# Kernel optimization log

Hardware: AMD Instinct MI355X
Metric: run time of the kernel (lower is better)

The kernel has to match this reference:

```python
import jax, jax.numpy as jnp
import numpy as np

N = 50000
E = 800000
F_IN = 64
F_OUT = 64


def setup_inputs() -> dict:
    key = jax.random.key(0)
    ks = jax.random.split(key, 14)
    x = jax.random.normal(ks[0], (N, F_IN), dtype=jnp.float32)
    row_low = jax.random.randint(ks[1], (E,), 0, N)
    col_low = jax.random.randint(ks[2], (E,), 0, N)
    val_low = jax.random.uniform(ks[3], (E,), dtype=jnp.float32)
    row_high = jax.random.randint(ks[4], (E,), 0, N)
    col_high = jax.random.randint(ks[5], (E,), 0, N)
    val_high = jax.random.uniform(ks[6], (E,), dtype=jnp.float32)
    # xavier-uniform style init for weights
    def xavier(k, shape):
        fan_in, fan_out = shape[0], shape[1]
        bound = float(np.sqrt(6.0 / (fan_in + fan_out)))
        return jax.random.uniform(k, shape, jnp.float32, -bound, bound)
    W_low = xavier(ks[7], (F_IN, F_OUT))
    W_high = xavier(ks[8], (F_IN, F_OUT))
    W_mlp = xavier(ks[9], (F_IN, F_OUT))
    a_low = xavier(ks[10], (F_OUT, 1))
    a_high = xavier(ks[11], (F_OUT, 1))
    a_mlp = xavier(ks[12], (F_OUT, 1))
    att3 = xavier(ks[13], (3, 3))
    return dict(x=x, row_low=row_low, col_low=col_low, val_low=val_low,
                row_high=row_high, col_high=col_high, val_high=val_high,
                W_low=W_low, W_high=W_high, W_mlp=W_mlp,
                a_low=a_low, a_high=a_high, a_mlp=a_mlp, att3=att3)


def _spmm(row, col, val, h, n):
    # (sparse adj) @ h : gather source rows, scale by edge weight, scatter-add to dest
    return jax.ops.segment_sum(val[:, None] * h[col], row, num_segments=n)


def reference(x, row_low, col_low, val_low, row_high, col_high, val_high,
              W_low, W_high, W_mlp, a_low, a_high, a_mlp, att3):
    n = x.shape[0]
    out_low = jax.nn.relu(_spmm(row_low, col_low, val_low, x @ W_low, n))
    out_high = jax.nn.relu(_spmm(row_high, col_high, val_high, x @ W_high, n))
    out_mlp = jax.nn.relu(x @ W_mlp)
    T = 3.0
    feats = jnp.concatenate([out_low @ a_low, out_high @ a_high, out_mlp @ a_mlp], axis=1)  # [N,3]
    logits = (jax.nn.sigmoid(feats) @ att3) / T
    att = jax.nn.softmax(logits, axis=1)  # [N,3]
    return 3.0 * (att[:, 0:1] * out_low + att[:, 1:2] * out_high + att[:, 2:3] * out_mlp)
```

## Files before the change

kernel.cpp:

```cpp
#include <hip/hip_runtime.h>
#include <hip/hip_fp16.h>


#define NNODE 50000
#define NEDGE 800000
#define NBUCK 782
#define CAP   1552

typedef __attribute__((ext_vector_type(8))) short short8v;
typedef __attribute__((ext_vector_type(4))) float float4v;

__device__ __forceinline__ unsigned short f2bf(float f) {
    unsigned u = __float_as_uint(f);
    u += 0x7FFFu + ((u >> 16) & 1u);
    return (unsigned short)(u >> 16);
}
__device__ __forceinline__ __half2 u_as_h2(unsigned u) {
    return *reinterpret_cast<__half2*>(&u);
}

__global__ __launch_bounds__(256)
void zero_kernel(unsigned int* __restrict__ g)
{
    const int i = blockIdx.x * 256 + threadIdx.x;
    if (i < 2 * NBUCK) g[i] = 0u;
}

__global__ __launch_bounds__(256)
void gemm_mfma_kernel(const float* __restrict__ x,
                      const float* __restrict__ Wl, const float* __restrict__ Wh,
                      const float* __restrict__ Wm,
                      unsigned short* __restrict__ hl16,
                      unsigned short* __restrict__ hh16,
                      unsigned short* __restrict__ hm16)
{
    __shared__ unsigned short wt[3][64][72];
    const int t = threadIdx.x;
#pragma unroll 1
    for (int m = 0; m < 3; ++m) {
        const float* __restrict__ W = (m == 0) ? Wl : (m == 1) ? Wh : Wm;
        for (int i = t; i < 4096; i += 256) {
            const int k = i >> 6, c = i & 63;
            wt[m][c][k] = f2bf(W[i]);
        }
    }
    __syncthreads();

    const int wid = t >> 6, lane = t & 63;
    const int node0 = blockIdx.x * 64 + wid * 16;
    if (node0 >= NNODE) return;
    const int arow = lane & 15;
    const int hi = lane >> 4;

    const float* __restrict__ xr = x + (size_t)(node0 + arow) * 64 + hi * 8;
    const float4 pa0 = *(const float4*)(xr + 0);
    const float4 pa1 = *(const float4*)(xr + 4);
    const float4 pb0 = *(const float4*)(xr + 32);
    const float4 pb1 = *(const float4*)(xr + 36);
    short8v a0, a1;
    a0[0] = (short)f2bf(pa0.x); a0[1] = (short)f2bf(pa0.y);
    a0[2] = (short)f2bf(pa0.z); a0[3] = (short)f2bf(pa0.w);
    a0[4] = (short)f2bf(pa1.x); a0[5] = (short)f2bf(pa1.y);
    a0[6] = (short)f2bf(pa1.z); a0[7] = (short)f2bf(pa1.w);
    a1[0] = (short)f2bf(pb0.x); a1[1] = (short)f2bf(pb0.y);
    a1[2] = (short)f2bf(pb0.z); a1[3] = (short)f2bf(pb0.w);
    a1[4] = (short)f2bf(pb1.x); a1[5] = (short)f2bf(pb1.y);
    a1[6] = (short)f2bf(pb1.z); a1[7] = (short)f2bf(pb1.w);

#pragma unroll 1
    for (int m = 0; m < 3; ++m) {
        unsigned short* __restrict__ H = (m == 0) ? hl16 : (m == 1) ? hh16 : hm16;
        float4v acc0 = {0.f, 0.f, 0.f, 0.f}, acc1 = {0.f, 0.f, 0.f, 0.f};
        float4v acc2 = {0.f, 0.f, 0.f, 0.f}, acc3 = {0.f, 0.f, 0.f, 0.f};

#define DO_CT(CT, ACC)                                                          \
        {                                                                       \
            const short8v b0 = *(const short8v*)&wt[m][CT * 16 + arow][hi * 8]; \
            const short8v b1 = *(const short8v*)&wt[m][CT * 16 + arow][32 + hi * 8]; \
            ACC = __builtin_amdgcn_mfma_f32_16x16x32_bf16(a0, b0, ACC, 0, 0, 0); \
            ACC = __builtin_amdgcn_mfma_f32_16x16x32_bf16(a1, b1, ACC, 0, 0, 0); \
        }
        DO_CT(0, acc0) DO_CT(1, acc1) DO_CT(2, acc2) DO_CT(3, acc3)
#undef DO_CT

        const bool rl = (m == 2);
#define ST_CT(CT, ACC)                                                          \
        {                                                                       \
            _Pragma("unroll")                                                   \
            for (int r = 0; r < 4; ++r) {                                       \
                float v = ACC[r];                                               \
                if (rl) v = fmaxf(v, 0.f);                                      \
                H[(size_t)(node0 + hi * 4 + r) * 64 + CT * 16 + arow] =         \
                    __half_as_ushort(__float2half(v));                          \
            }                                                                   \
        }
        ST_CT(0, acc0) ST_CT(1, acc1) ST_CT(2, acc2) ST_CT(3, acc3)
#undef ST_CT
    }
}

__global__ __launch_bounds__(512)
void scatter_kernel(const int* __restrict__ row_low, const int* __restrict__ col_low,
                    const float* __restrict__ val_low,
                    const int* __restrict__ row_high, const int* __restrict__ col_high,
                    const float* __restrict__ val_high,
                    unsigned int* __restrict__ gcursor, uint2* __restrict__ packed)
{
    __shared__ unsigned int hist_s[2 * NBUCK];
    __shared__ unsigned int base_s[2 * NBUCK];
    const int t = threadIdx.x;
    const int ebase = blockIdx.x * 8192;

    for (int i = t; i < 2 * NBUCK; i += 512) hist_s[i] = 0u;
    __syncthreads();

    int rows[16]; unsigned int rank[16];
#pragma unroll
    for (int j = 0; j < 16; ++j) {
        const int e = ebase + j * 512 + t;
        rows[j] = 0; rank[j] = 0u;
        if (e < 2 * NEDGE) {
            const int r = (e < NEDGE) ? row_low[e] : row_high[e - NEDGE];
            const int fb = ((e < NEDGE) ? 0 : NBUCK) + (r >> 6);
            rows[j] = r;
            rank[j] = atomicAdd(&hist_s[fb], 1u);
        }
    }
    __syncthreads();
    for (int i = t; i < 2 * NBUCK; i += 512) {
        const unsigned int c = hist_s[i];
        base_s[i] = c ? atomicAdd(&gcursor[i], c) : 0u;
    }
    __syncthreads();
#pragma unroll
    for (int j = 0; j < 16; ++j) {
        const int e = ebase + j * 512 + t;
        if (e < 2 * NEDGE) {
            const int g = (e >= NEDGE);
            const int ee = e - g * NEDGE;
            const int r = rows[j];
            const int c = g ? col_high[ee] : col_low[ee];
            const float v = g ? val_high[ee] : val_low[ee];
            const int fb = g * NBUCK + (r >> 6);
            const unsigned int pos = base_s[fb] + rank[j];
            if (pos < CAP) {
                const unsigned short hb = __half_as_ushort(__float2half(v));
                uint2 pk;
                pk.x = (unsigned int)c | ((unsigned int)(r & 63) << 16);
                pk.y = (unsigned)hb | ((unsigned)hb << 16);
                packed[(size_t)fb * CAP + pos] = pk;
            }
        }
    }
}

__global__ __launch_bounds__(256)
void sort_kernel(uint2* __restrict__ packed,
                 const unsigned int* __restrict__ gcursor,
                 int* __restrict__ rs, int* __restrict__ rc)
{
    __shared__ uint2 es[CAP];
    __shared__ unsigned int hist[64];
    __shared__ unsigned int offs[64];
    __shared__ unsigned int cur[64];

    const int fb = blockIdx.x;
    const int t = threadIdx.x;
    uint2* __restrict__ seg = packed + (size_t)fb * CAP;
    int cnt = (int)gcursor[fb];
    if (cnt > CAP) cnt = CAP;

    if (t < 64) { hist[t] = 0u; cur[t] = 0u; }
    __syncthreads();

    for (int i = t; i < cnt; i += 256) {
        const uint2 p = seg[i];
        es[i] = p;
        atomicAdd(&hist[(p.x >> 16) & 63u], 1u);
    }
    __syncthreads();

    if (t < 64) {
        const int pv = (int)((hist[t] + 7u) & ~7u);
        int xsc = pv;
#pragma unroll
        for (int d = 1; d < 64; d <<= 1) {
            int y = __shfl_up(xsc, d, 64);
            if (t >= d) xsc += y;
        }
        offs[t] = (unsigned)(xsc - pv);
    }
    __syncthreads();

    for (int i = t; i < cnt; i += 256) {
        const uint2 p = es[i];
        const unsigned r = (p.x >> 16) & 63u;
        const unsigned pos = offs[r] + atomicAdd(&cur[r], 1u);
        if (pos < CAP) seg[pos] = p;
    }
    if (t < 64) {
        const unsigned b = offs[t] + hist[t];
        const unsigned e = offs[t] + ((hist[t] + 7u) & ~7u);
        const uint2 z = {0u, 0u};
        for (unsigned u = b; u < e && u < CAP; ++u) seg[u] = z;
    }

    if (t < 64) {
        const int g = (fb >= NBUCK);
        const int node = ((fb - g * NBUCK) << 6) + t;
        if (node < NNODE) {
            const unsigned P = (hist[t] + 7u) & ~7u;
            const int avail = CAP - (int)offs[t];
            int nq = (int)(P >> 2);
            int nqa = avail > 0 ? ((avail >> 2) & ~1) : 0;
            if (nq > nqa) nq = nqa;
            rs[g * NNODE + node] = fb * CAP + (int)offs[t];
            rc[g * NNODE + node] = nq;
        }
    }
}

__global__ __launch_bounds__(256, 8)
void spmm_finalize_kernel(const uint2* __restrict__ packed,
                          const int* __restrict__ rs, const int* __restrict__ rc,
                          const unsigned short* __restrict__ hl16,
                          const unsigned short* __restrict__ hh16,
                          const unsigned short* __restrict__ hm16,
                          const float* __restrict__ aL, const float* __restrict__ aH,
                          const float* __restrict__ aM, const float* __restrict__ att3,
                          float* __restrict__ out)
{
    const int wid = threadIdx.x >> 6;
    const int lane = threadIdx.x & 63;
    const int sub = lane >> 4;
    const int f4 = (lane & 15) << 2;
    const unsigned fb2 = (unsigned)(f4 * 2);
    const int node = blockIdx.x * 4 + wid;
    if (node >= NNODE) return;

    const int sL = __builtin_amdgcn_readfirstlane(rs[node]);
    const int nqL = __builtin_amdgcn_readfirstlane(rc[node]);
    const int sH = __builtin_amdgcn_readfirstlane(rs[NNODE + node]);
    const int nqH = __builtin_amdgcn_readfirstlane(rc[NNODE + node]);
    const uint2* __restrict__ segL = packed + sL + sub;
    const uint2* __restrict__ segH = packed + sH + sub;
    const int nqm = (nqL > nqH) ? nqL : nqH;

    const __half2 hz2 = u_as_h2(0u);
    __half2 aL0a = hz2, aL1a = hz2, aL0b = hz2, aL1b = hz2;
    __half2 aH0a = hz2, aH1a = hz2, aH0b = hz2, aH1b = hz2;

    uint2 cL0 = segL[0], cL1 = segL[4];
    uint2 cH0 = segH[0], cH1 = segH[4];

#pragma unroll 1
    for (int q = 0; q < nqm; q += 2) {
        const uint2 nL0 = segL[q * 4 + 8],  nL1 = segL[q * 4 + 12];
        const uint2 nH0 = segH[q * 4 + 8],  nH1 = segH[q * 4 + 12];
        const uint2 uL0 = *(const uint2*)((const char*)hl16 + (size_t)(((cL0.x & 0xFFFFu) << 7) + fb2));
        const uint2 uL1 = *(const uint2*)((const char*)hl16 + (size_t)(((cL1.x & 0xFFFFu) << 7) + fb2));
        const uint2 uH0 = *(const uint2*)((const char*)hh16 + (size_t)(((cH0.x & 0xFFFFu) << 7) + fb2));
        const uint2 uH1 = *(const uint2*)((const char*)hh16 + (size_t)(((cH1.x & 0xFFFFu) << 7) + fb2));
        __builtin_amdgcn_sched_barrier(0);
        const __half2 vL0 = u_as_h2((q     < nqL) ? cL0.y : 0u);
        const __half2 vL1 = u_as_h2((q + 1 < nqL) ? cL1.y : 0u);
        const __half2 vH0 = u_as_h2((q     < nqH) ? cH0.y : 0u);
        const __half2 vH1 = u_as_h2((q + 1 < nqH) ? cH1.y : 0u);
        aL0a = __hfma2(u_as_h2(uL0.x), vL0, aL0a);
        aL1a = __hfma2(u_as_h2(uL0.y), vL0, aL1a);
        aL0b = __hfma2(u_as_h2(uL1.x), vL1, aL0b);
        aL1b = __hfma2(u_as_h2(uL1.y), vL1, aL1b);
        aH0a = __hfma2(u_as_h2(uH0.x), vH0, aH0a);
        aH1a = __hfma2(u_as_h2(uH0.y), vH0, aH1a);
        aH0b = __hfma2(u_as_h2(uH1.x), vH1, aH0b);
        aH1b = __hfma2(u_as_h2(uH1.y), vH1, aH1b);
        cL0 = nL0; cL1 = nL1; cH0 = nH0; cH1 = nH1;
    }

    float lx = __low2float(aL0a) + __low2float(aL0b);
    float ly = __high2float(aL0a) + __high2float(aL0b);
    float lz = __low2float(aL1a) + __low2float(aL1b);
    float lw = __high2float(aL1a) + __high2float(aL1b);
    float hx = __low2float(aH0a) + __low2float(aH0b);
    float hy = __high2float(aH0a) + __high2float(aH0b);
    float hz = __low2float(aH1a) + __low2float(aH1b);
    float hw = __high2float(aH1a) + __high2float(aH1b);

    lx += __shfl_xor(lx, 16, 64); ly += __shfl_xor(ly, 16, 64);
    lz += __shfl_xor(lz, 16, 64); lw += __shfl_xor(lw, 16, 64);
    hx += __shfl_xor(hx, 16, 64); hy += __shfl_xor(hy, 16, 64);
    hz += __shfl_xor(hz, 16, 64); hw += __shfl_xor(hw, 16, 64);
    lx += __shfl_xor(lx, 32, 64); ly += __shfl_xor(ly, 32, 64);
    lz += __shfl_xor(lz, 32, 64); lw += __shfl_xor(lw, 32, 64);
    hx += __shfl_xor(hx, 32, 64); hy += __shfl_xor(hy, 32, 64);
    hz += __shfl_xor(hz, 32, 64); hw += __shfl_xor(hw, 32, 64);

    const float olx = fmaxf(lx, 0.f), oly = fmaxf(ly, 0.f);
    const float olz = fmaxf(lz, 0.f), olw = fmaxf(lw, 0.f);
    const float ohx = fmaxf(hx, 0.f), ohy = fmaxf(hy, 0.f);
    const float ohz = fmaxf(hz, 0.f), ohw = fmaxf(hw, 0.f);

    const uint2 om2 = *(const uint2*)&hm16[(size_t)node * 64 + f4];
    const float omx = __low2float(u_as_h2(om2.x));
    const float omy = __high2float(u_as_h2(om2.x));
    const float omz = __low2float(u_as_h2(om2.y));
    const float omw = __high2float(u_as_h2(om2.y));

    const float4 aL4 = *(const float4*)&aL[f4];
    const float4 aH4 = *(const float4*)&aH[f4];
    const float4 aM4 = *(const float4*)&aM[f4];

    float f0 = olx * aL4.x + oly * aL4.y + olz * aL4.z + olw * aL4.w;
    float f1 = ohx * aH4.x + ohy * aH4.y + ohz * aH4.z + ohw * aH4.w;
    float f2 = omx * aM4.x + omy * aM4.y + omz * aM4.z + omw * aM4.w;
#pragma unroll
    for (int msk = 1; msk < 16; msk <<= 1) {
        f0 += __shfl_xor(f0, msk, 64);
        f1 += __shfl_xor(f1, msk, 64);
        f2 += __shfl_xor(f2, msk, 64);
    }
    const float s0 = 1.f / (1.f + __expf(-f0));
    const float s1 = 1.f / (1.f + __expf(-f1));
    const float s2 = 1.f / (1.f + __expf(-f2));
    const float invT = 1.f / 3.f;
    const float l0g = (s0 * att3[0] + s1 * att3[3] + s2 * att3[6]) * invT;
    const float l1g = (s0 * att3[1] + s1 * att3[4] + s2 * att3[7]) * invT;
    const float l2g = (s0 * att3[2] + s1 * att3[5] + s2 * att3[8]) * invT;
    const float mx = fmaxf(l0g, fmaxf(l1g, l2g));
    const float e0 = __expf(l0g - mx);
    const float e1 = __expf(l1g - mx);
    const float e2 = __expf(l2g - mx);
    const float inv = 1.f / (e0 + e1 + e2);
    const float wl = 3.f * inv * e0, wh = 3.f * inv * e1, wm = 3.f * inv * e2;

    if (lane < 16) {
        float4 o;
        o.x = wl * olx + wh * ohx + wm * omx;
        o.y = wl * oly + wh * ohy + wm * omy;
        o.z = wl * olz + wh * ohz + wm * omz;
        o.w = wl * olw + wh * ohw + wm * omw;
        *(float4*)&out[(size_t)node * 64 + f4] = o;
    }
}

extern "C" void kernel_launch(void* const* d_in, const int* in_sizes, int n_in,
                              void* d_out, int out_size, void* d_ws, size_t ws_size,
                              hipStream_t stream)
{
    const float* x        = (const float*)d_in[0];
    const int*   row_low  = (const int*)  d_in[1];
    const int*   col_low  = (const int*)  d_in[2];
    const float* val_low  = (const float*)d_in[3];
    const int*   row_high = (const int*)  d_in[4];
    const int*   col_high = (const int*)  d_in[5];
    const float* val_high = (const float*)d_in[6];
    const float* W_low    = (const float*)d_in[7];
    const float* W_high   = (const float*)d_in[8];
    const float* W_mlp    = (const float*)d_in[9];
    const float* a_low    = (const float*)d_in[10];
    const float* a_high   = (const float*)d_in[11];
    const float* a_mlp    = (const float*)d_in[12];
    const float* att3     = (const float*)d_in[13];
    float* out = (float*)d_out;

    const size_t NM = (size_t)NNODE * 64;

    unsigned short* hl16    = (unsigned short*)d_ws;
    unsigned short* hh16    = hl16 + NM;
    unsigned short* hm16    = hh16 + NM;
    uint2*          packed  = (uint2*)(hm16 + NM);
    unsigned int*   gcursor = (unsigned int*)(packed + (size_t)2 * NBUCK * CAP);
    int*            rs      = (int*)(gcursor + 2 * NBUCK);
    int*            rc      = rs + 2 * NNODE;

    zero_kernel<<<(2 * NBUCK + 255) / 256, 256, 0, stream>>>(gcursor);

    scatter_kernel<<<(2 * NEDGE + 8191) / 8192, 512, 0, stream>>>(
        row_low, col_low, val_low, row_high, col_high, val_high, gcursor, packed);

    gemm_mfma_kernel<<<(NNODE + 63) / 64, 256, 0, stream>>>(
        x, W_low, W_high, W_mlp, hl16, hh16, hm16);

    sort_kernel<<<2 * NBUCK, 256, 0, stream>>>(packed, gcursor, rs, rc);

    spmm_finalize_kernel<<<(NNODE + 3) / 4, 256, 0, stream>>>(
        packed, rs, rc, hl16, hh16, hm16, a_low, a_high, a_mlp, att3, out);
}
```

Baseline: 101.4 us.

## Shrink edge records to 4 bytes with separate row byte array

Edge records drop from 8 bytes (col+row, duplicated half value) to a 4-byte word packing the column and half-precision value, with the local row id kept in a separate byte array used only by the sort. This cuts memory traffic in scatter, sort and the SpMM gather loop, and halves the sort's shared-memory footprint. The SpMM loop also drops its explicit software prefetch of the next records and rebuilds the duplicated half2 value with a few ALU ops. Packing the column into 16 bits matches the old format, so it carries the same limit on node ids.

```diff
diff --git a/kernel.cpp b/kernel.cpp
--- a/kernel.cpp
+++ b/kernel.cpp
@@ -104,7 +104,9 @@
                     const float* __restrict__ val_low,
                     const int* __restrict__ row_high, const int* __restrict__ col_high,
                     const float* __restrict__ val_high,
-                    unsigned int* __restrict__ gcursor, uint2* __restrict__ packed)
+                    unsigned int* __restrict__ gcursor,
+                    unsigned int* __restrict__ rec4,
+                    unsigned char* __restrict__ row8)
 {
     __shared__ unsigned int hist_s[2 * NBUCK];
     __shared__ unsigned int base_s[2 * NBUCK];
@@ -145,28 +147,30 @@
             const unsigned int pos = base_s[fb] + rank[j];
             if (pos < CAP) {
                 const unsigned short hb = __half_as_ushort(__float2half(v));
-                uint2 pk;
-                pk.x = (unsigned int)c | ((unsigned int)(r & 63) << 16);
-                pk.y = (unsigned)hb | ((unsigned)hb << 16);
-                packed[(size_t)fb * CAP + pos] = pk;
+                const size_t slot = (size_t)fb * CAP + pos;
+                rec4[slot] = (unsigned)c | ((unsigned)hb << 16);
+                row8[slot] = (unsigned char)(r & 63);
             }
         }
     }
 }
 
 __global__ __launch_bounds__(256)
-void sort_kernel(uint2* __restrict__ packed,
+void sort_kernel(unsigned int* __restrict__ rec4,
+                 const unsigned char* __restrict__ row8,
                  const unsigned int* __restrict__ gcursor,
                  int* __restrict__ rs, int* __restrict__ rc)
 {
-    __shared__ uint2 es[CAP];
+    __shared__ unsigned int rec_s[CAP];
+    __shared__ unsigned char row_s[CAP];
     __shared__ unsigned int hist[64];
     __shared__ unsigned int offs[64];
     __shared__ unsigned int cur[64];
 
     const int fb = blockIdx.x;
     const int t = threadIdx.x;
-    uint2* __restrict__ seg = packed + (size_t)fb * CAP;
+    unsigned int* __restrict__ seg = rec4 + (size_t)fb * CAP;
+    const unsigned char* __restrict__ rseg = row8 + (size_t)fb * CAP;
     int cnt = (int)gcursor[fb];
     if (cnt > CAP) cnt = CAP;
 
@@ -174,9 +178,10 @@
     __syncthreads();
 
     for (int i = t; i < cnt; i += 256) {
-        const uint2 p = seg[i];
-        es[i] = p;
-        atomicAdd(&hist[(p.x >> 16) & 63u], 1u);
+        rec_s[i] = seg[i];
+        const unsigned char r = rseg[i];
+        row_s[i] = r;
+        atomicAdd(&hist[r], 1u);
     }
     __syncthreads();
 
@@ -193,16 +198,14 @@
     __syncthreads();
 
     for (int i = t; i < cnt; i += 256) {
-        const uint2 p = es[i];
-        const unsigned r = (p.x >> 16) & 63u;
+        const unsigned r = row_s[i];
         const unsigned pos = offs[r] + atomicAdd(&cur[r], 1u);
-        if (pos < CAP) seg[pos] = p;
+        if (pos < CAP) seg[pos] = rec_s[i];
     }
     if (t < 64) {
         const unsigned b = offs[t] + hist[t];
         const unsigned e = offs[t] + ((hist[t] + 7u) & ~7u);
-        const uint2 z = {0u, 0u};
-        for (unsigned u = b; u < e && u < CAP; ++u) seg[u] = z;
+        for (unsigned u = b; u < e && u < CAP; ++u) seg[u] = 0u;
     }
 
     if (t < 64) {
@@ -221,7 +224,7 @@
 }
 
 __global__ __launch_bounds__(256, 8)
-void spmm_finalize_kernel(const uint2* __restrict__ packed,
+void spmm_finalize_kernel(const unsigned int* __restrict__ rec4,
                           const int* __restrict__ rs, const int* __restrict__ rc,
                           const unsigned short* __restrict__ hl16,
                           const unsigned short* __restrict__ hh16,
@@ -242,30 +245,33 @@
     const int nqL = __builtin_amdgcn_readfirstlane(rc[node]);
     const int sH = __builtin_amdgcn_readfirstlane(rs[NNODE + node]);
     const int nqH = __builtin_amdgcn_readfirstlane(rc[NNODE + node]);
-    const uint2* __restrict__ segL = packed + sL + sub;
-    const uint2* __restrict__ segH = packed + sH + sub;
+    const unsigned int* __restrict__ segL = rec4 + sL + sub;
+    const unsigned int* __restrict__ segH = rec4 + sH + sub;
     const int nqm = (nqL > nqH) ? nqL : nqH;
 
     const __half2 hz2 = u_as_h2(0u);
     __half2 aL0a = hz2, aL1a = hz2, aL0b = hz2, aL1b = hz2;
     __half2 aH0a = hz2, aH1a = hz2, aH0b = hz2, aH1b = hz2;
 
-    uint2 cL0 = segL[0], cL1 = segL[4];
-    uint2 cH0 = segH[0], cH1 = segH[4];
-
 #pragma unroll 1
     for (int q = 0; q < nqm; q += 2) {
-        const uint2 nL0 = segL[q * 4 + 8],  nL1 = segL[q * 4 + 12];
-        const uint2 nH0 = segH[q * 4 + 8],  nH1 = segH[q * 4 + 12];
-        const uint2 uL0 = *(const uint2*)((const char*)hl16 + (size_t)(((cL0.x & 0xFFFFu) << 7) + fb2));
-        const uint2 uL1 = *(const uint2*)((const char*)hl16 + (size_t)(((cL1.x & 0xFFFFu) << 7) + fb2));
-        const uint2 uH0 = *(const uint2*)((const char*)hh16 + (size_t)(((cH0.x & 0xFFFFu) << 7) + fb2));
-        const uint2 uH1 = *(const uint2*)((const char*)hh16 + (size_t)(((cH1.x & 0xFFFFu) << 7) + fb2));
+        const unsigned rL0 = segL[q * 4];
+        const unsigned rL1 = segL[q * 4 + 4];
+        const unsigned rH0 = segH[q * 4];
+        const unsigned rH1 = segH[q * 4 + 4];
+        const uint2 uL0 = *(const uint2*)((const char*)hl16 + (size_t)(((rL0 & 0xFFFFu) << 7) + fb2));
+        const uint2 uL1 = *(const uint2*)((const char*)hl16 + (size_t)(((rL1 & 0xFFFFu) << 7) + fb2));
+        const uint2 uH0 = *(const uint2*)((const char*)hh16 + (size_t)(((rH0 & 0xFFFFu) << 7) + fb2));
+        const uint2 uH1 = *(const uint2*)((const char*)hh16 + (size_t)(((rH1 & 0xFFFFu) << 7) + fb2));
         __builtin_amdgcn_sched_barrier(0);
-        const __half2 vL0 = u_as_h2((q     < nqL) ? cL0.y : 0u);
-        const __half2 vL1 = u_as_h2((q + 1 < nqL) ? cL1.y : 0u);
-        const __half2 vH0 = u_as_h2((q     < nqH) ? cH0.y : 0u);
-        const __half2 vH1 = u_as_h2((q + 1 < nqH) ? cH1.y : 0u);
+        const unsigned dL0 = (rL0 & 0xFFFF0000u) | (rL0 >> 16);
+        const unsigned dL1 = (rL1 & 0xFFFF0000u) | (rL1 >> 16);
+        const unsigned dH0 = (rH0 & 0xFFFF0000u) | (rH0 >> 16);
+        const unsigned dH1 = (rH1 & 0xFFFF0000u) | (rH1 >> 16);
+        const __half2 vL0 = u_as_h2((q     < nqL) ? dL0 : 0u);
+        const __half2 vL1 = u_as_h2((q + 1 < nqL) ? dL1 : 0u);
+        const __half2 vH0 = u_as_h2((q     < nqH) ? dH0 : 0u);
+        const __half2 vH1 = u_as_h2((q + 1 < nqH) ? dH1 : 0u);
         aL0a = __hfma2(u_as_h2(uL0.x), vL0, aL0a);
         aL1a = __hfma2(u_as_h2(uL0.y), vL0, aL1a);
         aL0b = __hfma2(u_as_h2(uL1.x), vL1, aL0b);
@@ -274,7 +280,6 @@
         aH1a = __hfma2(u_as_h2(uH0.y), vH0, aH1a);
         aH0b = __hfma2(u_as_h2(uH1.x), vH1, aH0b);
         aH1b = __hfma2(u_as_h2(uH1.y), vH1, aH1b);
-        cL0 = nL0; cL1 = nL1; cH0 = nH0; cH1 = nH1;
     }
 
     float lx = __low2float(aL0a) + __low2float(aL0b);
@@ -364,25 +369,28 @@
     float* out = (float*)d_out;
 
     const size_t NM = (size_t)NNODE * 64;
+    const size_t NSLOT = (size_t)2 * NBUCK * CAP;
 
     unsigned short* hl16    = (unsigned short*)d_ws;
     unsigned short* hh16    = hl16 + NM;
     unsigned short* hm16    = hh16 + NM;
-    uint2*          packed  = (uint2*)(hm16 + NM);
-    unsigned int*   gcursor = (unsigned int*)(packed + (size_t)2 * NBUCK * CAP);
+    unsigned int*   rec4    = (unsigned int*)(hm16 + NM);
+    unsigned char*  row8    = (unsigned char*)(rec4 + NSLOT);
+    unsigned int*   gcursor = (unsigned int*)(row8 + ((NSLOT + 3) & ~size_t(3)));
     int*            rs      = (int*)(gcursor + 2 * NBUCK);
     int*            rc      = rs + 2 * NNODE;
 
     zero_kernel<<<(2 * NBUCK + 255) / 256, 256, 0, stream>>>(gcursor);
 
     scatter_kernel<<<(2 * NEDGE + 8191) / 8192, 512, 0, stream>>>(
-        row_low, col_low, val_low, row_high, col_high, val_high, gcursor, packed);
+        row_low, col_low, val_low, row_high, col_high, val_high,
+        gcursor, rec4, row8);
 
     gemm_mfma_kernel<<<(NNODE + 63) / 64, 256, 0, stream>>>(
         x, W_low, W_high, W_mlp, hl16, hh16, hm16);
 
-    sort_kernel<<<2 * NBUCK, 256, 0, stream>>>(packed, gcursor, rs, rc);
+    sort_kernel<<<2 * NBUCK, 256, 0, stream>>>(rec4, row8, gcursor, rs, rc);
 
     spmm_finalize_kernel<<<(NNODE + 3) / 4, 256, 0, stream>>>(
-        packed, rs, rc, hl16, hh16, hm16, a_low, a_high, a_mlp, att3, out);
-}
+        rec4, rs, rc, hl16, hh16, hm16, a_low, a_high, a_mlp, att3, out);
+}
```

Result: faster. 95.69 us (-5.6%).
